# Optimization experiments

Measured on AMD Instinct MI355X. Metric: run time of the kernel, lower is better.

The kernel has to match this reference:

```python
import jax, jax.numpy as jnp
import numpy as np

TWO_PI = 6.283185307179586
ALPHA_CLIP = 0.999

def setup_inputs() -> dict:
    key = jax.random.key(0)
    k1, k2, k3, k4 = jax.random.split(key, 4)
    N, H, W = 256, 512, 512
    xyz = jax.random.uniform(k1, (N, 2), jnp.float32, -1.0, 1.0)      # NDC centers in [-1,1]
    rotation = jax.random.normal(k2, (N, 1), jnp.float32)             # pre-sigmoid angle
    scaling = jax.random.uniform(k3, (N, 2), jnp.float32, 0.05, 0.5)  # inverse std (init 1/5)
    features_dc = jax.random.uniform(k4, (N, 3), jnp.float32)         # RGB in [0,1]
    opacity = jnp.ones((N, 1), jnp.float32)                            # buffer of ones
    background = jnp.ones((3,), jnp.float32)                           # white background
    return {"xyz": xyz, "rotation": rotation, "scaling": scaling,
            "features_dc": features_dc, "opacity": opacity,
            "background": background, "H": H, "W": W}

def _render(xyz, rotation, scaling, features_dc, opacity, background, H, W):
    N = xyz.shape[0]
    # Project NDC [-1,1] -> pixel coords (x,y)
    wh = jnp.array([W, H], jnp.float32)
    means = (xyz * 0.5 + 0.5) * wh                                    # [N,2]
    # Anisotropic 2D covariance: std = 1/|scaling| px, angle via sigmoid
    theta = jax.nn.sigmoid(rotation[:, 0]) * TWO_PI                   # [N]
    std = 1.0 / (jnp.abs(scaling) + 1e-6)                             # [N,2]
    s0, s1 = std[:, 0] ** 2, std[:, 1] ** 2
    c, s = jnp.cos(theta), jnp.sin(theta)
    # Sigma = R diag(s0,s1) R^T
    A = c * c * s0 + s * s * s1
    B = c * s * (s0 - s1)
    Cc = s * s * s0 + c * c * s1
    det = A * Cc - B * B + 1e-12
    ia, ib, ic = Cc / det, -B / det, A / det                          # conic (inverse cov)
    # Pixel centers, flattened P = H*W
    px = jnp.arange(W, dtype=jnp.float32) + 0.5
    py = jnp.arange(H, dtype=jnp.float32) + 0.5
    gx, gy = jnp.meshgrid(px, py)                                     # [H,W]
    gx, gy = gx.reshape(-1), gy.reshape(-1)                           # [P]
    dx = gx[None, :] - means[:, 0:1]                                  # [N,P]
    dy = gy[None, :] - means[:, 1:2]                                  # [N,P]
    power = -0.5 * (ia[:, None] * dx * dx + 2.0 * ib[:, None] * dx * dy
                    + ic[:, None] * dy * dy)                          # [N,P] <= 0
    alpha = jnp.minimum(opacity * jnp.exp(power), ALPHA_CLIP)         # [N,P]
    # Front-to-back alpha compositing in gaussian index order
    logs = jnp.log1p(-alpha)                                          # [N,P]
    csum = jnp.cumsum(logs, axis=0)
    T_excl = jnp.exp(jnp.concatenate([jnp.zeros((1, alpha.shape[1]), alpha.dtype),
                                      csum[:-1]], axis=0))            # transmittance before i
    weights = alpha * T_excl                                          # [N,P]
    T_final = jnp.exp(csum[-1])                                       # [P]
    img = jnp.einsum('np,nc->cp', weights, features_dc)               # [3,P]
    img = img + background[:, None] * T_final[None, :]
    return img.reshape(3, H, W)

def reference(xyz, rotation, scaling, features_dc, opacity, background, H, W):
    return _render(xyz, rotation, scaling, features_dc, opacity, background, H, W)
```

## Files before the change

kernel.cpp:

```cpp
#include <hip/hip_runtime.h>
#include <math.h>


#define BLOCK 256
#define QMAX 30.0f
#define ALPHA_CLIP 0.999f
#define LOG2E 1.4426950408889634f

__global__ __launch_bounds__(BLOCK) void render_kernel(
    const float* __restrict__ xyz,
    const float* __restrict__ rot,
    const float* __restrict__ scal,
    const float* __restrict__ feat,
    const float* __restrict__ opac,
    const float* __restrict__ bg,
    const int* __restrict__ dH,
    const int* __restrict__ dW,
    float* __restrict__ out,
    int N, int P)
{
    __shared__ float sg[BLOCK * 16];
    __shared__ int   list[BLOCK];
    __shared__ int   wcnt[BLOCK / 64];
    __shared__ int   sM;

    const int t = threadIdx.x;
    const int W = *dW, H = *dH;
    const int tiles_x = W >> 6;
    const int tx0 = (blockIdx.x % tiles_x) << 6;
    const int ty0 = (blockIdx.x / tiles_x) << 4;

    const float fx0 = (float)tx0, fx1 = (float)(tx0 + 64);
    const float fy0 = (float)ty0, fy1 = (float)(ty0 + 16);

    const float gxp  = fx0 + (float)(t & 63) + 0.5f;
    const float gyp0 = fy0 + (float)(t >> 6) + 0.5f;

    float T[4]  = {1.f, 1.f, 1.f, 1.f};
    float ar[4] = {0.f, 0.f, 0.f, 0.f};
    float ag[4] = {0.f, 0.f, 0.f, 0.f};
    float ab[4] = {0.f, 0.f, 0.f, 0.f};

    for (int c0 = 0; c0 < N; c0 += BLOCK) {
        const int i = c0 + t;
        bool pred = false;
        if (i < N) {
            const float Wf = (float)W, Hf = (float)H;
            const float mx = (xyz[2*i]   * 0.5f + 0.5f) * Wf;
            const float my = (xyz[2*i+1] * 0.5f + 0.5f) * Hf;
            const float r  = rot[i];
            const float theta = (1.0f / (1.0f + expf(-r))) * 6.283185307179586f;
            const float sd0 = 1.0f / (fabsf(scal[2*i])   + 1e-6f);
            const float sd1 = 1.0f / (fabsf(scal[2*i+1]) + 1e-6f);
            const float s0 = sd0 * sd0, s1 = sd1 * sd1;
            const float c = cosf(theta), s = sinf(theta);
            const float A  = c*c*s0 + s*s*s1;
            const float B  = c*s*(s0 - s1);
            const float Cc = s*s*s0 + c*c*s1;
            const float det = A*Cc - B*B + 1e-12f;
            const float inv = 1.0f / det;
            const float kk = -0.5f * LOG2E;
            const float rx = sqrtf(QMAX * A);
            const float ry = sqrtf(QMAX * Cc);

            float* rec = &sg[t * 16];
            rec[0]  = mx;
            rec[1]  = my;
            rec[2]  = Cc * inv * kk;
            rec[3]  = -B * inv * 2.0f * kk;
            rec[4]  = A  * inv * kk;
            rec[5]  = log2f(opac[i]);
            rec[6]  = feat[3*i+0];
            rec[7]  = feat[3*i+1];
            rec[8]  = feat[3*i+2];
            rec[12] = mx - rx;
            rec[13] = mx + rx;
            rec[14] = my - ry;
            rec[15] = my + ry;

            pred = (rec[13] >= fx0) & (rec[12] <= fx1) &
                   (rec[15] >= fy0) & (rec[14] <= fy1);
        }

        const unsigned long long m = __ballot(pred);
        const int lane = t & 63, wid = t >> 6;
        if (lane == 0) wcnt[wid] = __popcll(m);
        __syncthreads();
        int off = 0;
        for (int w = 0; w < wid; ++w) off += wcnt[w];
        if (pred)
            list[off + __popcll(m & ((1ull << lane) - 1ull))] = t;
        if (t == 0) sM = wcnt[0] + wcnt[1] + wcnt[2] + wcnt[3];
        __syncthreads();
        const int M = sM;

        for (int j = 0; j < M; ++j) {
            const int idx = list[j];
            const float* rec = &sg[idx * 16];
            const float4 g0 = *(const float4*)rec;
            const float4 g1 = *(const float4*)(rec + 4);
            const float  cb = rec[8];
            const float dx = gxp - g0.x;
            const float q0 = fmaf(g0.z * dx, dx, g1.y);
            const float bx = g0.w * dx;
#pragma unroll
            for (int k = 0; k < 4; ++k) {
                const float dy = (gyp0 + 4.0f * (float)k) - g0.y;
                const float ea = fmaf(dy, fmaf(g1.x, dy, bx), q0);
                const float alpha = fminf(exp2f(ea), ALPHA_CLIP);
                const float w = alpha * T[k];
                ar[k] = fmaf(w, g1.z, ar[k]);
                ag[k] = fmaf(w, g1.w, ag[k]);
                ab[k] = fmaf(w, cb, ab[k]);
                T[k] -= w;
            }
        }
        __syncthreads();
    }

    const float b0 = bg[0], b1 = bg[1], b2 = bg[2];
    const int px = tx0 + (t & 63);
#pragma unroll
    for (int k = 0; k < 4; ++k) {
        const int py = ty0 + (t >> 6) + 4 * k;
        if (px < W && py < H) {
            const int p = py * W + px;
            out[p]         = fmaf(b0, T[k], ar[k]);
            out[P + p]     = fmaf(b1, T[k], ag[k]);
            out[2*P + p]   = fmaf(b2, T[k], ab[k]);
        }
    }
}

extern "C" void kernel_launch(void* const* d_in, const int* in_sizes, int n_in,
                              void* d_out, int out_size, void* d_ws, size_t ws_size,
                              hipStream_t stream) {
    const float* xyz  = (const float*)d_in[0];
    const float* rot  = (const float*)d_in[1];
    const float* scal = (const float*)d_in[2];
    const float* feat = (const float*)d_in[3];
    const float* opac = (const float*)d_in[4];
    const float* bg   = (const float*)d_in[5];
    const int*   dH   = (const int*)d_in[6];
    const int*   dW   = (const int*)d_in[7];
    float* out = (float*)d_out;

    const int N = in_sizes[0] / 2;
    const int P = out_size / 3;

    const int blocks = (P + 1023) / 1024;
    render_kernel<<<blocks, BLOCK, 0, stream>>>(xyz, rot, scal, feat, opac, bg,
                                                dH, dW, out, N, P);
}
```

Measured before the change: 72.73 us.

## Halve tile height and compact culled gaussian records directly into shared memory

Tiles shrink from 64x16 to 64x8 pixels, so each thread handles 2 rows instead of 4 and the grid has twice as many blocks. The smaller tile bounding box culls gaussians more tightly and the extra blocks give more parallelism across CUs. Surviving gaussians are now written straight into a compacted shared-memory array with a 12-float stride, which removes the index list and its indirect lookup in the inner loop. In exchange, the per-gaussian setup and culling work is repeated across twice as many blocks.

```diff
diff --git a/kernel.cpp b/kernel.cpp
--- a/kernel.cpp
+++ b/kernel.cpp
@@ -6,6 +6,7 @@
 #define QMAX 30.0f
 #define ALPHA_CLIP 0.999f
 #define LOG2E 1.4426950408889634f
+#define RSTRIDE 12
 
 __global__ __launch_bounds__(BLOCK) void render_kernel(
     const float* __restrict__ xyz,
@@ -19,8 +20,7 @@
     float* __restrict__ out,
     int N, int P)
 {
-    __shared__ float sg[BLOCK * 16];
-    __shared__ int   list[BLOCK];
+    __shared__ float sg[BLOCK * RSTRIDE];
     __shared__ int   wcnt[BLOCK / 64];
     __shared__ int   sM;
 
@@ -28,26 +28,28 @@
     const int W = *dW, H = *dH;
     const int tiles_x = W >> 6;
     const int tx0 = (blockIdx.x % tiles_x) << 6;
-    const int ty0 = (blockIdx.x / tiles_x) << 4;
+    const int ty0 = (blockIdx.x / tiles_x) << 3;
 
     const float fx0 = (float)tx0, fx1 = (float)(tx0 + 64);
-    const float fy0 = (float)ty0, fy1 = (float)(ty0 + 16);
+    const float fy0 = (float)ty0, fy1 = (float)(ty0 + 8);
 
     const float gxp  = fx0 + (float)(t & 63) + 0.5f;
     const float gyp0 = fy0 + (float)(t >> 6) + 0.5f;
 
-    float T[4]  = {1.f, 1.f, 1.f, 1.f};
-    float ar[4] = {0.f, 0.f, 0.f, 0.f};
-    float ag[4] = {0.f, 0.f, 0.f, 0.f};
-    float ab[4] = {0.f, 0.f, 0.f, 0.f};
+    float T[2]  = {1.f, 1.f};
+    float ar[2] = {0.f, 0.f};
+    float ag[2] = {0.f, 0.f};
+    float ab[2] = {0.f, 0.f};
 
     for (int c0 = 0; c0 < N; c0 += BLOCK) {
         const int i = c0 + t;
         bool pred = false;
+        float mx = 0.f, my = 0.f, ia2 = 0.f, ib2 = 0.f, ic2 = 0.f;
+        float lop = 0.f, cr = 0.f, cg = 0.f, cb = 0.f;
         if (i < N) {
             const float Wf = (float)W, Hf = (float)H;
-            const float mx = (xyz[2*i]   * 0.5f + 0.5f) * Wf;
-            const float my = (xyz[2*i+1] * 0.5f + 0.5f) * Hf;
+            mx = (xyz[2*i]   * 0.5f + 0.5f) * Wf;
+            my = (xyz[2*i+1] * 0.5f + 0.5f) * Hf;
             const float r  = rot[i];
             const float theta = (1.0f / (1.0f + expf(-r))) * 6.283185307179586f;
             const float sd0 = 1.0f / (fabsf(scal[2*i])   + 1e-6f);
@@ -63,23 +65,16 @@
             const float rx = sqrtf(QMAX * A);
             const float ry = sqrtf(QMAX * Cc);
 
-            float* rec = &sg[t * 16];
-            rec[0]  = mx;
-            rec[1]  = my;
-            rec[2]  = Cc * inv * kk;
-            rec[3]  = -B * inv * 2.0f * kk;
-            rec[4]  = A  * inv * kk;
-            rec[5]  = log2f(opac[i]);
-            rec[6]  = feat[3*i+0];
-            rec[7]  = feat[3*i+1];
-            rec[8]  = feat[3*i+2];
-            rec[12] = mx - rx;
-            rec[13] = mx + rx;
-            rec[14] = my - ry;
-            rec[15] = my + ry;
+            ia2 = Cc * inv * kk;
+            ib2 = -B * inv * 2.0f * kk;
+            ic2 = A  * inv * kk;
+            lop = log2f(opac[i]);
+            cr  = feat[3*i+0];
+            cg  = feat[3*i+1];
+            cb  = feat[3*i+2];
 
-            pred = (rec[13] >= fx0) & (rec[12] <= fx1) &
-                   (rec[15] >= fy0) & (rec[14] <= fy1);
+            pred = (mx + rx >= fx0) & (mx - rx <= fx1) &
+                   (my + ry >= fy0) & (my - ry <= fy1);
         }
 
         const unsigned long long m = __ballot(pred);
@@ -88,30 +83,34 @@
         __syncthreads();
         int off = 0;
         for (int w = 0; w < wid; ++w) off += wcnt[w];
-        if (pred)
-            list[off + __popcll(m & ((1ull << lane) - 1ull))] = t;
+        if (pred) {
+            const int pos = off + __popcll(m & ((1ull << lane) - 1ull));
+            float* rec = &sg[pos * RSTRIDE];
+            ((float4*)rec)[0] = make_float4(mx, my, ia2, ib2);
+            ((float4*)rec)[1] = make_float4(ic2, lop, cr, cg);
+            rec[8] = cb;
+        }
         if (t == 0) sM = wcnt[0] + wcnt[1] + wcnt[2] + wcnt[3];
         __syncthreads();
         const int M = sM;
 
         for (int j = 0; j < M; ++j) {
-            const int idx = list[j];
-            const float* rec = &sg[idx * 16];
+            const float* rec = &sg[j * RSTRIDE];
             const float4 g0 = *(const float4*)rec;
             const float4 g1 = *(const float4*)(rec + 4);
-            const float  cb = rec[8];
+            const float  fb = rec[8];
             const float dx = gxp - g0.x;
             const float q0 = fmaf(g0.z * dx, dx, g1.y);
             const float bx = g0.w * dx;
 #pragma unroll
-            for (int k = 0; k < 4; ++k) {
+            for (int k = 0; k < 2; ++k) {
                 const float dy = (gyp0 + 4.0f * (float)k) - g0.y;
                 const float ea = fmaf(dy, fmaf(g1.x, dy, bx), q0);
                 const float alpha = fminf(exp2f(ea), ALPHA_CLIP);
                 const float w = alpha * T[k];
                 ar[k] = fmaf(w, g1.z, ar[k]);
                 ag[k] = fmaf(w, g1.w, ag[k]);
-                ab[k] = fmaf(w, cb, ab[k]);
+                ab[k] = fmaf(w, fb, ab[k]);
                 T[k] -= w;
             }
         }
@@ -121,7 +120,7 @@
     const float b0 = bg[0], b1 = bg[1], b2 = bg[2];
     const int px = tx0 + (t & 63);
 #pragma unroll
-    for (int k = 0; k < 4; ++k) {
+    for (int k = 0; k < 2; ++k) {
         const int py = ty0 + (t >> 6) + 4 * k;
         if (px < W && py < H) {
             const int p = py * W + px;
@@ -148,7 +147,7 @@
     const int N = in_sizes[0] / 2;
     const int P = out_size / 3;
 
-    const int blocks = (P + 1023) / 1024;
+    const int blocks = (P + 511) / 512;
     render_kernel<<<blocks, BLOCK, 0, stream>>>(xyz, rot, scal, feat, opac, bg,
                                                 dH, dW, out, N, P);
 }
```

After: 70.76 us. 2.7% less time.
